# Performance work log

Measured on AMD Instinct MI355X. Metric: run time of the kernel, lower is better.

The kernel has to match this reference:

```python
import jax, jax.numpy as jnp
import numpy as np

EPS = 1e-5

def conv1d_same(x, w, b):
    # x: [B,C,T], w: [O,I,K], b: [O]
    y = jax.lax.conv_general_dilated(x, w, window_strides=(1,), padding='SAME',
                                     dimension_numbers=('NCH', 'OIH', 'NCH'))
    return y + b[None, :, None]

def bn_eval(x, gamma, beta):
    # running_mean=0, running_var=1 (fresh BatchNorm1d in eval mode)
    inv = 1.0 / jnp.sqrt(1.0 + EPS)
    return x * (gamma * inv)[None, :, None] + beta[None, :, None]

def gelu(x):
    return jax.nn.gelu(x, approximate=False)

def conv_block(x, c1w, c1b, c2w, c2b, g1, be1, g2, be2, skw=None, skb=None):
    res = x if skw is None else jnp.einsum('bct,oc->bot', x, skw[:, :, 0]) + skb[None, :, None]
    h = gelu(bn_eval(conv1d_same(x, c1w, c1b), g1, be1))
    h = bn_eval(conv1d_same(h, c2w, c2b), g2, be2)
    return gelu(h + res)

def setup_inputs() -> dict:
    key = jax.random.key(0)
    ks = jax.random.split(key, 32)
    B, C, T = 1024, 271, 281
    H, H2, E, NCLS, NSUBJ = 128, 256, 16, 1854, 4
    g = lambda i, shape, s=0.02: jax.random.normal(ks[i], shape, dtype=jnp.float32) * s
    inp = {}
    inp['X'] = jax.random.normal(ks[0], (B, C, T), dtype=jnp.float32)
    inp['subject_idxs'] = jax.random.randint(ks[1], (B,), 0, NSUBJ, dtype=jnp.int32)
    inp['attention'] = jax.random.normal(ks[2], (C, C), dtype=jnp.float32)
    inp['sa_w'] = g(3, (H, C), 0.05)
    inp['sa_b'] = jnp.zeros((H,), jnp.float32)
    inp['subj_w'] = g(4, (NSUBJ, H, H), 0.05)
    inp['subj_b'] = jnp.zeros((NSUBJ, H), jnp.float32)
    # block1: 128->128 (identity skip)
    inp['b1_c1w'] = g(5, (H, H, 3)); inp['b1_c1b'] = jnp.zeros((H,), jnp.float32)
    inp['b1_c2w'] = g(6, (H, H, 3)); inp['b1_c2b'] = jnp.zeros((H,), jnp.float32)
    inp['b1_g1'] = jnp.ones((H,), jnp.float32); inp['b1_be1'] = jnp.zeros((H,), jnp.float32)
    inp['b1_g2'] = jnp.ones((H,), jnp.float32); inp['b1_be2'] = jnp.zeros((H,), jnp.float32)
    # block2: 128->256 (1x1 conv skip)
    inp['b2_c1w'] = g(7, (H2, H, 3)); inp['b2_c1b'] = jnp.zeros((H2,), jnp.float32)
    inp['b2_c2w'] = g(8, (H2, H2, 3)); inp['b2_c2b'] = jnp.zeros((H2,), jnp.float32)
    inp['b2_g1'] = jnp.ones((H2,), jnp.float32); inp['b2_be1'] = jnp.zeros((H2,), jnp.float32)
    inp['b2_g2'] = jnp.ones((H2,), jnp.float32); inp['b2_be2'] = jnp.zeros((H2,), jnp.float32)
    inp['b2_skw'] = g(9, (H2, H, 1)); inp['b2_skb'] = jnp.zeros((H2,), jnp.float32)
    # block3: 256->256 (identity skip)
    inp['b3_c1w'] = g(10, (H2, H2, 3)); inp['b3_c1b'] = jnp.zeros((H2,), jnp.float32)
    inp['b3_c2w'] = g(11, (H2, H2, 3)); inp['b3_c2b'] = jnp.zeros((H2,), jnp.float32)
    inp['b3_g1'] = jnp.ones((H2,), jnp.float32); inp['b3_be1'] = jnp.zeros((H2,), jnp.float32)
    inp['b3_g2'] = jnp.ones((H2,), jnp.float32); inp['b3_be2'] = jnp.zeros((H2,), jnp.float32)
    # subject embedding + head
    inp['emb'] = g(12, (NSUBJ, E), 1.0)
    inp['head_w1'] = g(13, (H, H2 + E), 0.05); inp['head_b1'] = jnp.zeros((H,), jnp.float32)
    inp['head_w2'] = g(14, (NCLS, H), 0.05); inp['head_b2'] = jnp.zeros((NCLS,), jnp.float32)
    return inp

def reference(X, subject_idxs, attention, sa_w, sa_b, subj_w, subj_b,
              b1_c1w, b1_c1b, b1_c2w, b1_c2b, b1_g1, b1_be1, b1_g2, b1_be2,
              b2_c1w, b2_c1b, b2_c2w, b2_c2b, b2_g1, b2_be1, b2_g2, b2_be2, b2_skw, b2_skb,
              b3_c1w, b3_c1b, b3_c2w, b3_c2b, b3_g1, b3_be1, b3_g2, b3_be2,
              emb, head_w1, head_b1, head_w2, head_b2):
    # SpatialAttention
    attn = jax.nn.softmax(attention, axis=1)            # [C,C]
    x = jnp.einsum('bct,ic->bit', X, attn)              # [B,C,T]
    x = jnp.einsum('bit,oi->bot', x, sa_w) + sa_b[None, :, None]  # [B,H,T]
    # Per-subject 1x1 conv: batched gather of weights instead of python loop
    Ws = subj_w[subject_idxs]                           # [B,H,H]
    bs = subj_b[subject_idxs]                           # [B,H]
    x = jnp.einsum('bct,boc->bot', x, Ws) + bs[:, :, None]
    # ConvBlock stack
    x = conv_block(x, b1_c1w, b1_c1b, b1_c2w, b1_c2b, b1_g1, b1_be1, b1_g2, b1_be2)
    x = conv_block(x, b2_c1w, b2_c1b, b2_c2w, b2_c2b, b2_g1, b2_be1, b2_g2, b2_be2, b2_skw, b2_skb)
    x = conv_block(x, b3_c1w, b3_c1b, b3_c2w, b3_c2b, b3_g1, b3_be1, b3_g2, b3_be2)
    # Head: global avg pool over time, concat subject embedding, MLP
    x = jnp.mean(x, axis=2)                             # [B,2H]
    x = jnp.concatenate([x, emb[subject_idxs]], axis=1) # [B,2H+E]
    h = jax.nn.relu(x @ head_w1.T + head_b1)
    return h @ head_w2.T + head_b2                      # [B,num_classes]
```

## Files before the change

kernel.cpp:

```cpp
#include <hip/hip_runtime.h>
#include <hip/hip_bf16.h>
#include <math.h>

constexpr int Bz = 1024;
constexpr int C0 = 271;
constexpr int CP0 = 288;
constexpr int Tt = 281;
constexpr int TR = 292;
constexpr int H1 = 128;
constexpr int H2 = 256;
constexpr int NCLS = 1854;
constexpr int ED = 16;
constexpr float BN_INV = 0.9999950000374996f;

typedef __attribute__((ext_vector_type(8))) short s16x8;
typedef __attribute__((ext_vector_type(16))) float f32x16;

__device__ __forceinline__ float gelu_f(float v) {
    return 0.5f * v * (1.0f + erff(v * 0.7071067811865475f));
}
__device__ __forceinline__ float bf2f(short s) {
    return __builtin_bit_cast(float, ((unsigned int)(unsigned short)s) << 16);
}
__device__ __forceinline__ short f2bf(float f) {
    return __builtin_bit_cast(short, __float2bfloat16(f));
}

typedef unsigned int u32;
typedef const __attribute__((address_space(1))) u32 gu32;
typedef __attribute__((address_space(3))) u32 lu32;

__device__ __forceinline__ void gl16(const void* g, void* l) {
    __builtin_amdgcn_global_load_lds((gu32*)(uintptr_t)g, (lu32*)(uintptr_t)l, 16, 0, 0);
}
template<int N> __device__ __forceinline__ void waitv() {
    asm volatile("s_waitcnt vmcnt(%0)" :: "i"(N) : "memory");
}
__device__ __forceinline__ void hard_barrier() {
    __builtin_amdgcn_s_barrier();
    __builtin_amdgcn_sched_barrier(0);
}


__global__ void zrows_k(short* base, int C) {
    const int b = blockIdx.x;
    const int n = 11 * (C / 8);
    for (int i = threadIdx.x; i < n; i += 256) {
        int ri = i / (C / 8), c8 = i - ri * (C / 8);
        int row = (ri == 0) ? 0 : 281 + ri;
        *(int4*)(base + ((size_t)b * TR + row) * C + c8 * 8) = make_int4(0, 0, 0, 0);
    }
}

__global__ void softmax_rows_k(const float* __restrict__ a, float* __restrict__ o, int n) {
    __shared__ float red[256];
    const int row = blockIdx.x, tid = threadIdx.x;
    const float* r = a + (size_t)row * n;
    float m = -1e30f;
    for (int i = tid; i < n; i += 256) m = fmaxf(m, r[i]);
    red[tid] = m; __syncthreads();
    for (int s = 128; s > 0; s >>= 1) { if (tid < s) red[tid] = fmaxf(red[tid], red[tid + s]); __syncthreads(); }
    m = red[0]; __syncthreads();
    float acc = 0.f;
    for (int i = tid; i < n; i += 256) acc += expf(r[i] - m);
    red[tid] = acc; __syncthreads();
    for (int s = 128; s > 0; s >>= 1) { if (tid < s) red[tid] += red[tid + s]; __syncthreads(); }
    const float inv = 1.0f / red[0];
    for (int i = tid; i < n; i += 256) o[(size_t)row * n + i] = expf(r[i] - m) * inv;
}

__global__ void gemm_M_k(const float* __restrict__ sa_w, const float* __restrict__ attnS,
                         float* __restrict__ M) {
    int idx = blockIdx.x * 256 + threadIdx.x;
    if (idx >= H1 * C0) return;
    int o = idx / C0, c = idx - o * C0;
    float s = 0.f;
    for (int i = 0; i < C0; ++i) s = fmaf(sa_w[(size_t)o * C0 + i], attnS[(size_t)i * C0 + c], s);
    M[idx] = s;
}

__global__ void wfrag_k(const float* __restrict__ w, short* __restrict__ out,
                        int CIN, int O, int K, int NC) {
    int idx = blockIdx.x * 256 + threadIdx.x;
    int OB32 = O / 32;
    int total = NC * K * OB32 * 2 * 512;
    if (idx >= total) return;
    int j = idx & 7, lane = (idx >> 3) & 63, kk = (idx >> 9) & 1, r = idx >> 10;
    int ob = r % OB32, r2 = r / OB32;
    int k = r2 % K, cc = r2 / K;
    int o = ob * 32 + (lane & 31);
    int c = cc * 32 + kk * 16 + (lane >> 5) * 8 + j;
    float v = (c < CIN) ? w[((size_t)o * CIN + c) * K + k] : 0.f;
    out[idx] = f2bf(v);
}

__global__ void msubA_k(const float* __restrict__ subj_w, const float* __restrict__ M,
                        short* __restrict__ out) {
    int idx = blockIdx.x * 256 + threadIdx.x;
    const int per_s = 9 * 1 * 4 * 2 * 512;
    if (idx >= 4 * per_s) return;
    int s = idx / per_s, rem = idx % per_s;
    int j = rem & 7, lane = (rem >> 3) & 63, kk = (rem >> 9) & 1, r = rem >> 10;
    int ob = r % 4, cc = r / 4;
    int o = ob * 32 + (lane & 31);
    int c = cc * 32 + kk * 16 + (lane >> 5) * 8 + j;
    float a = 0.f;
    if (c < C0) {
        const float* wr = subj_w + ((size_t)s * 128 + o) * 128;
        for (int h = 0; h < 128; ++h) a = fmaf(wr[h], M[(size_t)h * C0 + c], a);
    }
    out[idx] = f2bf(a);
}

__global__ void biasS_k(const float* __restrict__ subj_w, const float* __restrict__ sa_b,
                        const float* __restrict__ subj_b, float* __restrict__ biasS) {
    int idx = blockIdx.x * 256 + threadIdx.x;
    if (idx >= 4 * H1) return;
    int s = idx >> 7, o = idx & 127;
    const float* wr = subj_w + ((size_t)s * H1 + o) * H1;
    float a = subj_b[idx];
    for (int h = 0; h < H1; ++h) a = fmaf(wr[h], sa_b[h], a);
    biasS[idx] = a;
}

__global__ void xpose_k(const float* __restrict__ X, short* __restrict__ xT) {
    __shared__ float tile[32][33];
    int b = blockIdx.z;
    int t0 = blockIdx.x * 32, c0 = blockIdx.y * 32;
    int tx = threadIdx.x, ty = threadIdx.y;
    #pragma unroll
    for (int i = 0; i < 4; ++i) {
        int c = c0 + ty + i * 8, t = t0 + tx;
        float v = 0.f;
        if (c < C0 && t < Tt) v = X[((size_t)b * C0 + c) * Tt + t];
        tile[ty + i * 8][tx] = v;
    }
    __syncthreads();
    #pragma unroll
    for (int i = 0; i < 4; ++i) {
        int t = t0 + ty + i * 8, c = c0 + tx;
        if (t < Tt) xT[((size_t)b * TR + t + 1) * CP0 + c] = f2bf(tile[tx][ty + i * 8]);
    }
}


template<int K, int NC, int O_BLK, int NOW, int NB, bool GELU, bool HASRES>
__global__ __launch_bounds__(NOW * NB * 192)
void convMF(const short* __restrict__ xin, int XC,
            const short* __restrict__ wfrag,
            const float* __restrict__ bias,
            const float* __restrict__ gamma, const float* __restrict__ beta,
            const short* __restrict__ res, short* __restrict__ out,
            const int* __restrict__ sidx, int wsub, int bsub)
{
    constexpr int NW     = NOW * NB * 3;
    constexpr int NT     = NW * 64;
    constexpr int OB32   = O_BLK / 32;
    constexpr int PAD    = (K - 1) / 2;
    constexpr int RSTART = 1 - PAD;
    constexpr int A_I    = K * OB32 * 2;
    constexpr int X_I    = 18;
    constexpr int TI     = A_I + NB * X_I;
    constexpr int Q      = TI / NW;
    constexpr int R      = TI % NW;
    constexpr int QH     = (R > 0) ? Q + 1 : Q;
    constexpr int ABYTES = A_I * 1024;
    constexpr int X_SLOT = X_I * 1024 + 256;
    constexpr int HALF   = ABYTES + NB * X_SLOT;
    constexpr int O2     = O_BLK * 2;

    __shared__ __align__(16) char smem[2 * HALF];

    const int b0   = blockIdx.x * NB;
    const int tid  = threadIdx.x;
    const int lane = tid & 63, wv = tid >> 6;
    const int l31  = lane & 31, hi = lane >> 5;
    const int bqw  = wv / (NOW * 3);
    const int w2   = wv % (NOW * 3);
    const int wvt  = w2 / NOW;
    const int wvo  = w2 % NOW;
    const int tg   = wvt * 96;
    const int Sw   = Q + (wv < R ? 1 : 0);

    int subj = sidx ? sidx[b0] : 0;
    const char*  wbase = (const char*)(wfrag + (size_t)subj * wsub);
    const float* bb    = bias + (size_t)subj * bsub;

    f32x16 acc[2][3];
    #pragma unroll
    for (int i = 0; i < 2; ++i)
        #pragma unroll
        for (int j = 0; j < 3; ++j)
            #pragma unroll
            for (int e = 0; e < 16; ++e) acc[i][j][e] = 0.f;

    auto issue = [&](int cc, int pb) {
        char* base = smem + pb * HALF;
        const char* wsrc = wbase + (size_t)cc * (A_I * 1024);
        for (int s = 0; s < Sw; ++s) {
            int i = s * NW + wv;
            if (i < A_I) {
                gl16(wsrc + (size_t)i * 1024 + lane * 16, base + i * 1024);
            } else {
                int xi = i - A_I;
                int bql = xi / X_I, seg = xi - bql * X_I;
                int q = seg * 64 + lane;
                int r = q >> 2, p = q & 3;
                int ps = p ^ ((r >> 1) & 3);
                const char* g = (const char*)xin +
                    (((size_t)(b0 + bql) * TR + (RSTART + r)) * XC + cc * 32) * 2 + ps * 16;
                gl16(g, base + ABYTES + bql * X_SLOT + seg * 1024);
            }
        }
    };

    issue(0, 0);
    int cur = 0;
    for (int cc = 0; cc < NC; ++cc) {
        if (cc + 1 < NC) {
            issue(cc + 1, cur ^ 1);
            if (wv < R) waitv<QH>(); else waitv<Q>();
        } else {
            waitv<0>();
        }
        hard_barrier();

        const char* Ab = smem + cur * HALF;
        const char* Xb = Ab + ABYTES + bqw * X_SLOT;
        #pragma unroll
        for (int k = 0; k < K; ++k) {
            #pragma unroll
            for (int kk = 0; kk < 2; ++kk) {
                s16x8 a0 = *(const s16x8*)(Ab + (((k * OB32 + wvo * 2 + 0) * 2 + kk) << 10) + (lane << 4));
                s16x8 a1 = *(const s16x8*)(Ab + (((k * OB32 + wvo * 2 + 1) * 2 + kk) << 10) + (lane << 4));
                #pragma unroll
                for (int ts = 0; ts < 3; ++ts) {
                    int rl = tg + ts * 32 + l31 + k;
                    s16x8 bv = *(const s16x8*)(Xb + rl * 64 + ((((kk << 1) | hi) ^ ((rl >> 1) & 3)) << 4));
                    acc[0][ts] = __builtin_amdgcn_mfma_f32_32x32x16_bf16(a0, bv, acc[0][ts], 0, 0, 0);
                    acc[1][ts] = __builtin_amdgcn_mfma_f32_32x32x16_bf16(a1, bv, acc[1][ts], 0, 0, 0);
                }
            }
        }
        hard_barrier();
        cur ^= 1;
    }

    constexpr int RCH = O_BLK / 8;
    for (int g = 0; g < 3; ++g) {
        __syncthreads();
        if (wvt == g) {
            #pragma unroll
            for (int os = 0; os < 2; ++os) {
                #pragma unroll
                for (int rq = 0; rq < 4; ++rq) {
                    #pragma unroll
                    for (int rp = 0; rp < 2; ++rp) {
                        const int oc = wvo * 64 + os * 32 + 8 * rq + rp * 2 + 4 * hi;
                        const float bv0 = bb[oc], bv1 = bb[oc + 1];
                        const float g0 = gamma ? gamma[oc] * BN_INV : 1.f;
                        const float g1 = gamma ? gamma[oc + 1] * BN_INV : 1.f;
                        const float e0 = beta ? beta[oc] : 0.f;
                        const float e1 = beta ? beta[oc + 1] : 0.f;
                        const int r0 = rq * 4 + rp * 2;
                        #pragma unroll
                        for (int ts = 0; ts < 3; ++ts) {
                            float v0 = (acc[os][ts][r0] + bv0) * g0 + e0;
                            float v1 = (acc[os][ts][r0 + 1] + bv1) * g1 + e1;
                            int tl = ts * 32 + l31;
                            int byte = (bqw * 96 + tl) * O2 + ((oc * 2) ^ ((tl & 15) << 4));
                            __hip_bfloat162 pk;
                            pk.x = __float2bfloat16(v0);
                            pk.y = __float2bfloat16(v1);
                            *(__hip_bfloat162*)(smem + byte) = pk;
                        }
                    }
                }
            }
        }
        __syncthreads();
        for (int qq = tid; qq < NB * 96 * RCH; qq += NT) {
            int bql = qq / (96 * RCH), rem = qq - bql * (96 * RCH);
            int r = rem / RCH, cp = rem - r * RCH;
            int t = g * 96 + r;
            if (t >= Tt) continue;
            s16x8 hv = *(const s16x8*)(smem + (bql * 96 + r) * O2 + ((cp * 16) ^ ((r & 15) << 4)));
            size_t orow = ((size_t)(b0 + bql) * TR + t + 1) * O_BLK + cp * 8;
            s16x8 rv;
            if (HASRES) rv = *(const s16x8*)(res + orow);
            s16x8 ov;
            #pragma unroll
            for (int j = 0; j < 8; ++j) {
                float v = bf2f(hv[j]);
                if (HASRES) v += bf2f(rv[j]);
                if (GELU) v = gelu_f(v);
                ov[j] = f2bf(v);
            }
            *(s16x8*)(out + orow) = ov;
        }
    }
}


__global__ void poolCL_k(const short* __restrict__ x, float* __restrict__ pooled) {
    const int b = blockIdx.x;
    const int o = threadIdx.x;
    const short* p = x + ((size_t)b * TR + 1) * H2 + o;
    float s = 0.f;
    for (int t = 0; t < Tt; ++t) s += bf2f(p[(size_t)t * H2]);
    pooled[(size_t)b * H2 + o] = s * (1.0f / Tt);
}

__global__ void head1_k(const float* __restrict__ pooled, const float* __restrict__ emb,
                        const int* __restrict__ sidx, const float* __restrict__ w1,
                        const float* __restrict__ b1, float* __restrict__ hout) {
    int idx = blockIdx.x * 256 + threadIdx.x;
    if (idx >= Bz * H1) return;
    int b = idx >> 7, j = idx & 127;
    const float* wr = w1 + (size_t)j * (H2 + ED);
    const float* pr = pooled + (size_t)b * H2;
    float a = b1[j];
    for (int i = 0; i < H2; ++i) a = fmaf(pr[i], wr[i], a);
    const float* er = emb + (size_t)sidx[b] * ED;
    #pragma unroll
    for (int e = 0; e < ED; ++e) a = fmaf(er[e], wr[H2 + e], a);
    hout[idx] = fmaxf(a, 0.f);
}

__global__ __launch_bounds__(256)
void head2_k(const float* __restrict__ h, const float* __restrict__ w2,
             const float* __restrict__ b2, float* __restrict__ out) {
    const int n0 = blockIdx.x * 64;
    const int b0 = blockIdx.y * 16;
    __shared__ float hs[16][128];
    __shared__ float w2s[64][129];
    const int tid = threadIdx.x;
    for (int idx = tid; idx < 16 * 128; idx += 256) {
        int bl = idx >> 7, j = idx & 127;
        hs[bl][j] = h[(size_t)(b0 + bl) * H1 + j];
    }
    for (int idx = tid; idx < 64 * 128; idx += 256) {
        int nl = idx >> 7, j = idx & 127;
        int n = n0 + nl;
        w2s[nl][j] = (n < NCLS) ? w2[(size_t)n * H1 + j] : 0.f;
    }
    __syncthreads();
    const int nl = tid & 63, bg = tid >> 6;
    float acc[4] = {0.f, 0.f, 0.f, 0.f};
    for (int j = 0; j < 128; ++j) {
        const float wv = w2s[nl][j];
        #pragma unroll
        for (int bb = 0; bb < 4; ++bb) acc[bb] = fmaf(wv, hs[bg * 4 + bb][j], acc[bb]);
    }
    const int n = n0 + nl;
    if (n < NCLS) {
        const float bv = b2[n];
        #pragma unroll
        for (int bb = 0; bb < 4; ++bb)
            out[(size_t)(b0 + bg * 4 + bb) * NCLS + n] = acc[bb] + bv;
    }
}


extern "C" void kernel_launch(void* const* d_in, const int* in_sizes, int n_in,
                              void* d_out, int out_size, void* d_ws, size_t ws_size,
                              hipStream_t stream) {
    const float* X      = (const float*)d_in[0];
    const int*   sidx   = (const int*)  d_in[1];
    const float* attn   = (const float*)d_in[2];
    const float* sa_w   = (const float*)d_in[3];
    const float* sa_b   = (const float*)d_in[4];
    const float* subj_w = (const float*)d_in[5];
    const float* subj_b = (const float*)d_in[6];
    const float* b1c1w = (const float*)d_in[7];  const float* b1c1b = (const float*)d_in[8];
    const float* b1c2w = (const float*)d_in[9];  const float* b1c2b = (const float*)d_in[10];
    const float* b1g1  = (const float*)d_in[11]; const float* b1be1 = (const float*)d_in[12];
    const float* b1g2  = (const float*)d_in[13]; const float* b1be2 = (const float*)d_in[14];
    const float* b2c1w = (const float*)d_in[15]; const float* b2c1b = (const float*)d_in[16];
    const float* b2c2w = (const float*)d_in[17]; const float* b2c2b = (const float*)d_in[18];
    const float* b2g1  = (const float*)d_in[19]; const float* b2be1 = (const float*)d_in[20];
    const float* b2g2  = (const float*)d_in[21]; const float* b2be2 = (const float*)d_in[22];
    const float* b2skw = (const float*)d_in[23]; const float* b2skb = (const float*)d_in[24];
    const float* b3c1w = (const float*)d_in[25]; const float* b3c1b = (const float*)d_in[26];
    const float* b3c2w = (const float*)d_in[27]; const float* b3c2b = (const float*)d_in[28];
    const float* b3g1  = (const float*)d_in[29]; const float* b3be1 = (const float*)d_in[30];
    const float* b3g2  = (const float*)d_in[31]; const float* b3be2 = (const float*)d_in[32];
    const float* emb   = (const float*)d_in[33];
    const float* hw1   = (const float*)d_in[34]; const float* hb1 = (const float*)d_in[35];
    const float* hw2   = (const float*)d_in[36]; const float* hb2 = (const float*)d_in[37];
    float* out = (float*)d_out;
    (void)in_sizes; (void)n_in; (void)out_size; (void)ws_size;

    char* wsp = (char*)d_ws;
    size_t off = 0;
    auto allocF = [&](size_t n) {
        float* p = (float*)(wsp + off);
        off += ((n * sizeof(float)) + 255) & ~(size_t)255;
        return p;
    };
    auto allocS = [&](size_t n) {
        short* p = (short*)(wsp + off);
        off += ((n * sizeof(short)) + 255) & ~(size_t)255;
        return p;
    };
    float* attnS   = allocF((size_t)C0 * C0);
    float* Mmat    = allocF((size_t)H1 * C0);
    float* biasS   = allocF((size_t)4 * H1);
    float* pooled  = allocF((size_t)Bz * H2);
    float* hbuf    = allocF((size_t)Bz * H1);
    short* wStageA = allocS((size_t)4 * 9 * 4 * 2 * 512);
    short* wp_b1c1 = allocS((size_t)4 * 3 * 4 * 2 * 512);
    short* wp_b1c2 = allocS((size_t)4 * 3 * 4 * 2 * 512);
    short* wp_skip = allocS((size_t)4 * 1 * 8 * 2 * 512);
    short* wp_b2c1 = allocS((size_t)4 * 3 * 8 * 2 * 512);
    short* wp_b2c2 = allocS((size_t)8 * 3 * 8 * 2 * 512);
    short* wp_b3c1 = allocS((size_t)8 * 3 * 8 * 2 * 512);
    short* wp_b3c2 = allocS((size_t)8 * 3 * 8 * 2 * 512);
    short* xT   = allocS((size_t)Bz * TR * CP0);
    short* bufP = allocS((size_t)Bz * TR * H1);
    short* bufQ = allocS((size_t)Bz * TR * H1);
    short* bufR = allocS((size_t)Bz * TR * H2);
    short* bufS = allocS((size_t)Bz * TR * H2);

    zrows_k<<<Bz, 256, 0, stream>>>(xT, CP0);
    zrows_k<<<Bz, 256, 0, stream>>>(bufP, H1);
    zrows_k<<<Bz, 256, 0, stream>>>(bufQ, H1);
    zrows_k<<<Bz, 256, 0, stream>>>(bufR, H2);
    zrows_k<<<Bz, 256, 0, stream>>>(bufS, H2);

    softmax_rows_k<<<C0, 256, 0, stream>>>(attn, attnS, C0);
    gemm_M_k<<<(H1 * C0 + 255) / 256, 256, 0, stream>>>(sa_w, attnS, Mmat);
    msubA_k<<<(4 * 36864 + 255) / 256, 256, 0, stream>>>(subj_w, Mmat, wStageA);
    biasS_k<<<2, 256, 0, stream>>>(subj_w, sa_b, subj_b, biasS);
    wfrag_k<<<(4*3*4*2*512 + 255) / 256, 256, 0, stream>>>(b1c1w, wp_b1c1, 128, 128, 3, 4);
    wfrag_k<<<(4*3*4*2*512 + 255) / 256, 256, 0, stream>>>(b1c2w, wp_b1c2, 128, 128, 3, 4);
    wfrag_k<<<(4*1*8*2*512 + 255) / 256, 256, 0, stream>>>(b2skw, wp_skip, 128, 256, 1, 4);
    wfrag_k<<<(4*3*8*2*512 + 255) / 256, 256, 0, stream>>>(b2c1w, wp_b2c1, 128, 256, 3, 4);
    wfrag_k<<<(8*3*8*2*512 + 255) / 256, 256, 0, stream>>>(b2c2w, wp_b2c2, 256, 256, 3, 8);
    wfrag_k<<<(8*3*8*2*512 + 255) / 256, 256, 0, stream>>>(b3c1w, wp_b3c1, 256, 256, 3, 8);
    wfrag_k<<<(8*3*8*2*512 + 255) / 256, 256, 0, stream>>>(b3c2w, wp_b3c2, 256, 256, 3, 8);
    xpose_k<<<dim3(9, 9, Bz), dim3(32, 8), 0, stream>>>(X, xT);

    convMF<1, 9, 128, 2, 1, false, false><<<Bz, 384, 0, stream>>>(
        xT, CP0, wStageA, biasS, nullptr, nullptr, nullptr, bufP, sidx, 36864, 128);
    convMF<3, 4, 128, 2, 2, true, false><<<Bz / 2, 768, 0, stream>>>(
        bufP, H1, wp_b1c1, b1c1b, b1g1, b1be1, nullptr, bufQ, nullptr, 0, 0);
    convMF<3, 4, 128, 2, 2, true, true><<<Bz / 2, 768, 0, stream>>>(
        bufQ, H1, wp_b1c2, b1c2b, b1g2, b1be2, bufP, bufP, nullptr, 0, 0);
    convMF<1, 4, 256, 4, 1, false, false><<<Bz, 768, 0, stream>>>(
        bufP, H1, wp_skip, b2skb, nullptr, nullptr, nullptr, bufS, nullptr, 0, 0);
    convMF<3, 4, 256, 4, 1, true, false><<<Bz, 768, 0, stream>>>(
        bufP, H1, wp_b2c1, b2c1b, b2g1, b2be1, nullptr, bufR, nullptr, 0, 0);
    convMF<3, 8, 256, 4, 1, true, true><<<Bz, 768, 0, stream>>>(
        bufR, H2, wp_b2c2, b2c2b, b2g2, b2be2, bufS, bufS, nullptr, 0, 0);
    convMF<3, 8, 256, 4, 1, true, false><<<Bz, 768, 0, stream>>>(
        bufS, H2, wp_b3c1, b3c1b, b3g1, b3be1, nullptr, bufR, nullptr, 0, 0);
    convMF<3, 8, 256, 4, 1, true, true><<<Bz, 768, 0, stream>>>(
        bufR, H2, wp_b3c2, b3c2b, b3g2, b3be2, bufS, bufS, nullptr, 0, 0);

    poolCL_k<<<Bz, 256, 0, stream>>>(bufS, pooled);
    head1_k<<<(Bz * H1 + 255) / 256, 256, 0, stream>>>(pooled, emb, sidx, hw1, hb1, hbuf);
    head2_k<<<dim3((NCLS + 63) / 64, Bz / 16), 256, 0, stream>>>(hbuf, hw2, hb2, out);
}
```

Measured before the change: 1.333 ms.

## Stage full input slab in LDS once and read weight fragments from global

The conv kernel no longer double-buffers 32-channel chunks of weights and activations through LDS. It now loads the whole per-sample input slab (all channels, all time rows) into LDS in one go, or in two phases for the 288-channel first layer. Weight fragments are read straight from global memory (cache) into registers for each channel chunk. This removes the per-chunk barriers and pipeline bookkeeping and uses a wider XOR swizzle, but it drops the overlap between loading and compute and may raise LDS use per block, which can lower occupancy.

```diff
diff --git a/kernel.cpp b/kernel.cpp
--- a/kernel.cpp
+++ b/kernel.cpp
@@ -144,32 +144,75 @@
 }
 
 
-template<int K, int NC, int O_BLK, int NOW, int NB, bool GELU, bool HASRES>
+template<int NCCp, int ROWUp, int NW, int NCH>
+__device__ __forceinline__ void convFS_stage(
+    const short* slabg, int XC, int cubase, char* lds, int wv, int lane)
+{
+    constexpr int ROWB = ROWUp * 16;
+    for (int i = wv; i < NCH; i += NW) {
+        int pos = i * 1024 + lane * 16;
+        int rl = pos / ROWB;
+        int up = (pos - rl * ROWB) >> 4;
+        if (rl > 291) rl = 291;
+        int ul = up ^ (rl & 7);
+        int srcu = (ul < NCCp * 4) ? ul : 0;
+        gl16(slabg + (size_t)rl * XC + (cubase + srcu) * 8, lds + i * 1024);
+    }
+}
+
+template<int K, int NCCp, int ROWUp, int OB32>
+__device__ __forceinline__ void convFS_compute(
+    f32x16 (&acc)[2][3], const short* __restrict__ wb, const char* Xb,
+    int ccbase, int tg, int lane, int l31, int hi, int wvo)
+{
+    constexpr int ROWB = ROWUp * 16;
+    constexpr int ROFF = 1 - (K - 1) / 2;
+    #pragma unroll
+    for (int cc = 0; cc < NCCp; ++cc) {
+        s16x8 a[2][K][2];
+        #pragma unroll
+        for (int os = 0; os < 2; ++os)
+            #pragma unroll
+            for (int k = 0; k < K; ++k)
+                #pragma unroll
+                for (int kk = 0; kk < 2; ++kk) {
+                    int ci = (((ccbase + cc) * K + k) * OB32 + wvo * 2 + os) * 2 + kk;
+                    a[os][k][kk] = *(const s16x8*)(wb + (size_t)ci * 512 + lane * 8);
+                }
+        #pragma unroll
+        for (int k = 0; k < K; ++k)
+            #pragma unroll
+            for (int kk = 0; kk < 2; ++kk)
+                #pragma unroll
+                for (int ts = 0; ts < 3; ++ts) {
+                    int rl = tg + ts * 32 + l31 + k + ROFF;
+                    s16x8 bv = *(const s16x8*)(Xb + (size_t)rl * ROWB +
+                        (((cc * 4 + (kk << 1) + hi) ^ (rl & 7)) << 4));
+                    acc[0][ts] = __builtin_amdgcn_mfma_f32_32x32x16_bf16(a[0][k][kk], bv, acc[0][ts], 0, 0, 0);
+                    acc[1][ts] = __builtin_amdgcn_mfma_f32_32x32x16_bf16(a[1][k][kk], bv, acc[1][ts], 0, 0, 0);
+                }
+    }
+}
+
+template<int K, int NCC_A, int ROWU_A, int NCC_B, int ROWU_B,
+         int O_BLK, int NOW, int NB, bool GELU, bool HASRES>
 __global__ __launch_bounds__(NOW * NB * 192)
-void convMF(const short* __restrict__ xin, int XC,
+void convFS(const short* __restrict__ xin, int XC,
             const short* __restrict__ wfrag,
             const float* __restrict__ bias,
             const float* __restrict__ gamma, const float* __restrict__ beta,
             const short* __restrict__ res, short* __restrict__ out,
             const int* __restrict__ sidx, int wsub, int bsub)
 {
-    constexpr int NW     = NOW * NB * 3;
-    constexpr int NT     = NW * 64;
-    constexpr int OB32   = O_BLK / 32;
-    constexpr int PAD    = (K - 1) / 2;
-    constexpr int RSTART = 1 - PAD;
-    constexpr int A_I    = K * OB32 * 2;
-    constexpr int X_I    = 18;
-    constexpr int TI     = A_I + NB * X_I;
-    constexpr int Q      = TI / NW;
-    constexpr int R      = TI % NW;
-    constexpr int QH     = (R > 0) ? Q + 1 : Q;
-    constexpr int ABYTES = A_I * 1024;
-    constexpr int X_SLOT = X_I * 1024 + 256;
-    constexpr int HALF   = ABYTES + NB * X_SLOT;
-    constexpr int O2     = O_BLK * 2;
-
-    __shared__ __align__(16) char smem[2 * HALF];
+    constexpr int NW    = NOW * NB * 3;
+    constexpr int NT    = NW * 64;
+    constexpr int OB32  = O_BLK / 32;
+    constexpr int SLABB = ((292 * ROWU_A * 16) + 1023) & ~1023;
+    constexpr int NCH_A = SLABB / 1024;
+    constexpr int NCH_B = (292 * ROWU_B * 16 + 1023) / 1024;
+    constexpr int O2    = O_BLK * 2;
+
+    __shared__ __align__(16) char smem[NB * SLABB];
 
     const int b0   = blockIdx.x * NB;
     const int tid  = threadIdx.x;
@@ -180,11 +223,10 @@
     const int wvt  = w2 / NOW;
     const int wvo  = w2 % NOW;
     const int tg   = wvt * 96;
-    const int Sw   = Q + (wv < R ? 1 : 0);
 
     int subj = sidx ? sidx[b0] : 0;
-    const char*  wbase = (const char*)(wfrag + (size_t)subj * wsub);
-    const float* bb    = bias + (size_t)subj * bsub;
+    const short* wb = wfrag + (size_t)subj * wsub;
+    const float* bb = bias + (size_t)subj * bsub;
 
     f32x16 acc[2][3];
     #pragma unroll
@@ -194,56 +236,25 @@
             #pragma unroll
             for (int e = 0; e < 16; ++e) acc[i][j][e] = 0.f;
 
-    auto issue = [&](int cc, int pb) {
-        char* base = smem + pb * HALF;
-        const char* wsrc = wbase + (size_t)cc * (A_I * 1024);
-        for (int s = 0; s < Sw; ++s) {
-            int i = s * NW + wv;
-            if (i < A_I) {
-                gl16(wsrc + (size_t)i * 1024 + lane * 16, base + i * 1024);
-            } else {
-                int xi = i - A_I;
-                int bql = xi / X_I, seg = xi - bql * X_I;
-                int q = seg * 64 + lane;
-                int r = q >> 2, p = q & 3;
-                int ps = p ^ ((r >> 1) & 3);
-                const char* g = (const char*)xin +
-                    (((size_t)(b0 + bql) * TR + (RSTART + r)) * XC + cc * 32) * 2 + ps * 16;
-                gl16(g, base + ABYTES + bql * X_SLOT + seg * 1024);
-            }
-        }
-    };
-
-    issue(0, 0);
-    int cur = 0;
-    for (int cc = 0; cc < NC; ++cc) {
-        if (cc + 1 < NC) {
-            issue(cc + 1, cur ^ 1);
-            if (wv < R) waitv<QH>(); else waitv<Q>();
-        } else {
-            waitv<0>();
-        }
+    #pragma unroll
+    for (int b = 0; b < NB; ++b)
+        convFS_stage<NCC_A, ROWU_A, NW, NCH_A>(
+            xin + (size_t)(b0 + b) * TR * XC, XC, 0, smem + b * SLABB, wv, lane);
+    waitv<0>();
+    hard_barrier();
+
+    const char* Xb = smem + bqw * SLABB;
+    convFS_compute<K, NCC_A, ROWU_A, OB32>(acc, wb, Xb, 0, tg, lane, l31, hi, wvo);
+
+    if constexpr (NCC_B > 0) {
         hard_barrier();
-
-        const char* Ab = smem + cur * HALF;
-        const char* Xb = Ab + ABYTES + bqw * X_SLOT;
-        #pragma unroll
-        for (int k = 0; k < K; ++k) {
-            #pragma unroll
-            for (int kk = 0; kk < 2; ++kk) {
-                s16x8 a0 = *(const s16x8*)(Ab + (((k * OB32 + wvo * 2 + 0) * 2 + kk) << 10) + (lane << 4));
-                s16x8 a1 = *(const s16x8*)(Ab + (((k * OB32 + wvo * 2 + 1) * 2 + kk) << 10) + (lane << 4));
-                #pragma unroll
-                for (int ts = 0; ts < 3; ++ts) {
-                    int rl = tg + ts * 32 + l31 + k;
-                    s16x8 bv = *(const s16x8*)(Xb + rl * 64 + ((((kk << 1) | hi) ^ ((rl >> 1) & 3)) << 4));
-                    acc[0][ts] = __builtin_amdgcn_mfma_f32_32x32x16_bf16(a0, bv, acc[0][ts], 0, 0, 0);
-                    acc[1][ts] = __builtin_amdgcn_mfma_f32_32x32x16_bf16(a1, bv, acc[1][ts], 0, 0, 0);
-                }
-            }
-        }
+        #pragma unroll
+        for (int b = 0; b < NB; ++b)
+            convFS_stage<NCC_B, ROWU_B, NW, NCH_B>(
+                xin + (size_t)(b0 + b) * TR * XC, XC, NCC_A * 4, smem + b * SLABB, wv, lane);
+        waitv<0>();
         hard_barrier();
-        cur ^= 1;
+        convFS_compute<K, NCC_B, ROWU_B, OB32>(acc, wb, Xb, NCC_A, tg, lane, l31, hi, wvo);
     }
 
     constexpr int RCH = O_BLK / 8;
@@ -441,21 +452,21 @@
     wfrag_k<<<(8*3*8*2*512 + 255) / 256, 256, 0, stream>>>(b3c2w, wp_b3c2, 256, 256, 3, 8);
     xpose_k<<<dim3(9, 9, Bz), dim3(32, 8), 0, stream>>>(X, xT);
 
-    convMF<1, 9, 128, 2, 1, false, false><<<Bz, 384, 0, stream>>>(
+    convFS<1, 5, 24, 4, 16, 128, 2, 1, false, false><<<Bz, 384, 0, stream>>>(
         xT, CP0, wStageA, biasS, nullptr, nullptr, nullptr, bufP, sidx, 36864, 128);
-    convMF<3, 4, 128, 2, 2, true, false><<<Bz / 2, 768, 0, stream>>>(
+    convFS<3, 4, 16, 0, 0, 128, 2, 2, true, false><<<Bz / 2, 768, 0, stream>>>(
         bufP, H1, wp_b1c1, b1c1b, b1g1, b1be1, nullptr, bufQ, nullptr, 0, 0);
-    convMF<3, 4, 128, 2, 2, true, true><<<Bz / 2, 768, 0, stream>>>(
+    convFS<3, 4, 16, 0, 0, 128, 2, 2, true, true><<<Bz / 2, 768, 0, stream>>>(
         bufQ, H1, wp_b1c2, b1c2b, b1g2, b1be2, bufP, bufP, nullptr, 0, 0);
-    convMF<1, 4, 256, 4, 1, false, false><<<Bz, 768, 0, stream>>>(
+    convFS<1, 4, 16, 0, 0, 256, 4, 1, false, false><<<Bz, 768, 0, stream>>>(
         bufP, H1, wp_skip, b2skb, nullptr, nullptr, nullptr, bufS, nullptr, 0, 0);
-    convMF<3, 4, 256, 4, 1, true, false><<<Bz, 768, 0, stream>>>(
+    convFS<3, 4, 16, 0, 0, 256, 4, 1, true, false><<<Bz, 768, 0, stream>>>(
         bufP, H1, wp_b2c1, b2c1b, b2g1, b2be1, nullptr, bufR, nullptr, 0, 0);
-    convMF<3, 8, 256, 4, 1, true, true><<<Bz, 768, 0, stream>>>(
+    convFS<3, 8, 32, 0, 0, 256, 4, 1, true, true><<<Bz, 768, 0, stream>>>(
         bufR, H2, wp_b2c2, b2c2b, b2g2, b2be2, bufS, bufS, nullptr, 0, 0);
-    convMF<3, 8, 256, 4, 1, true, false><<<Bz, 768, 0, stream>>>(
+    convFS<3, 8, 32, 0, 0, 256, 4, 1, true, false><<<Bz, 768, 0, stream>>>(
         bufS, H2, wp_b3c1, b3c1b, b3g1, b3be1, nullptr, bufR, nullptr, 0, 0);
-    convMF<3, 8, 256, 4, 1, true, true><<<Bz, 768, 0, stream>>>(
+    convFS<3, 8, 32, 0, 0, 256, 4, 1, true, true><<<Bz, 768, 0, stream>>>(
         bufR, H2, wp_b3c2, b3c2b, b3g2, b3be2, bufS, bufS, nullptr, 0, 0);
 
     poolCL_k<<<Bz, 256, 0, stream>>>(bufS, pooled);
```

Result: slower. 1.370 ms (+2.8%).
